# Kernel optimization log

Hardware: AMD Instinct MI355X
Metric: run time of the kernel (lower is better)

The kernel has to match this reference:

```python
import jax, jax.numpy as jnp
import numpy as np

# Layer sizes for each 3-layer LSTM tower (input_dim, hidden_dim), as in the torch module.
SIZES = [(50, 25), (25, 10), (10, 4)]
B = 32768


def _lstm(x, Wih, Whh, b):
    """Single-layer batch-first LSTM (torch gate order i,f,g,o). x: [B,T,Din].
    Returns (ys [B,T,H], h_last [B,H]). b = b_ih + b_hh combined."""
    Bn = x.shape[0]
    H = Whh.shape[1]

    def step(carry, xt):
        h, c = carry
        gates = xt @ Wih.T + h @ Whh.T + b  # [B, 4H]
        i, f, g, o = jnp.split(gates, 4, axis=-1)
        c = jax.nn.sigmoid(f) * c + jax.nn.sigmoid(i) * jnp.tanh(g)
        h = jax.nn.sigmoid(o) * jnp.tanh(c)
        return (h, c), h

    z = jnp.zeros((Bn, H), x.dtype)
    (h_last, _), ys = jax.lax.scan(step, (z, z), jnp.swapaxes(x, 0, 1))
    return jnp.swapaxes(ys, 0, 1), h_last


def _tower(x, params):
    h = None
    for (Wih, Whh, b) in params:
        x, h = _lstm(x, Wih, Whh, b)
    return h  # last layer's final hidden state [B, 4]


def setup_inputs() -> dict:
    key = jax.random.key(0)
    inp = {}
    k_q, k_p, key = jax.random.split(key, 3)
    inp["q"] = jax.random.normal(k_q, (B, 12, 50), jnp.float32)
    inp["p"] = jax.random.normal(k_p, (B, 50, 50), jnp.float32)
    for prefix in ("q", "p"):
        for i, (din, dh) in enumerate(SIZES):
            k1, k2, key = jax.random.split(key, 3)
            inp[f"{prefix}Wih{i}"] = jax.random.normal(k1, (4 * dh, din), jnp.float32) * (1.0 / np.sqrt(din))
            inp[f"{prefix}Whh{i}"] = jax.random.normal(k2, (4 * dh, dh), jnp.float32) * (1.0 / np.sqrt(dh))
            inp[f"{prefix}b{i}"] = jnp.zeros((4 * dh,), jnp.float32)
    k1, key = jax.random.split(key)
    inp["fW"] = jax.random.normal(k1, (2, 4), jnp.float32) * 0.5
    inp["fb"] = jnp.zeros((2,), jnp.float32)
    return inp


def reference(q, p,
              qWih0, qWhh0, qb0, qWih1, qWhh1, qb1, qWih2, qWhh2, qb2,
              pWih0, pWhh0, pb0, pWih1, pWhh1, pb1, pWih2, pWhh2, pb2,
              fW, fb):
    q_params = [(qWih0, qWhh0, qb0), (qWih1, qWhh1, qb1), (qWih2, qWhh2, qb2)]
    p_params = [(pWih0, pWhh0, pb0), (pWih1, pWhh1, pb1), (pWih2, pWhh2, pb2)]
    h_q = _tower(q, q_params)  # [B, 4]
    h_p = _tower(p, p_params)  # [B, 4]
    scores = h_q * h_p
    return jax.nn.softmax(scores @ fW.T + fb, axis=1)  # [B, 2]
```

## Files before the change

kernel.cpp:

```cpp
#include <hip/hip_runtime.h>
#include <cstddef>

#define DEV static __device__ __forceinline__

constexpr int B_TOTAL = 32768;
constexpr int ROWS = 128;
constexpr int NBLK = B_TOTAL / ROWS;

constexpr int WL1_OFF = 7800, WL2_OFF = 9400, W_TOTAL = 9656;
constexpr int H0_STR = 28;
constexpr int H1_STR = 12;
constexpr int HQ_OFF = 0;
constexpr int HP_OFF = B_TOTAL * 4;

DEV float fexp2(float x) { return __builtin_amdgcn_exp2f(x); }
DEV float frcp(float x) { return __builtin_amdgcn_rcpf(x); }
DEV float fsig(float x) { return frcp(1.0f + fexp2(-1.4426950408889634f * x)); }
DEV float ftanh_(float x) { return 2.0f * frcp(1.0f + fexp2(-2.8853900817779268f * x)) - 1.0f; }

DEV float elem4(const float4 v, const int jj) {
  return jj == 0 ? v.x : jj == 1 ? v.y : jj == 2 ? v.z : v.w;
}

template <int NU>
DEV void gfma(float* __restrict__ g0, float* __restrict__ g1,
              const float4* __restrict__ w, const float va, const float vb) {
#pragma unroll
  for (int u = 0; u < NU; ++u) {
    const float4 wv = w[u];
    g0[4 * u + 0] = fmaf(wv.x, va, g0[4 * u + 0]);
    g0[4 * u + 1] = fmaf(wv.y, va, g0[4 * u + 1]);
    g0[4 * u + 2] = fmaf(wv.z, va, g0[4 * u + 2]);
    g0[4 * u + 3] = fmaf(wv.w, va, g0[4 * u + 3]);
    g1[4 * u + 0] = fmaf(wv.x, vb, g1[4 * u + 0]);
    g1[4 * u + 1] = fmaf(wv.y, vb, g1[4 * u + 1]);
    g1[4 * u + 2] = fmaf(wv.z, vb, g1[4 * u + 2]);
    g1[4 * u + 3] = fmaf(wv.w, vb, g1[4 * u + 3]);
  }
}

template <int NU>
DEV void activ(const float* __restrict__ g, float* __restrict__ c,
               float* __restrict__ hn) {
#pragma unroll
  for (int u = 0; u < NU; ++u) {
    const float gi_ = fsig(g[4 * u + 0]);
    const float gf  = fsig(g[4 * u + 1]);
    const float gg  = ftanh_(g[4 * u + 2]);
    const float go  = fsig(g[4 * u + 3]);
    const float cn  = fmaf(gf, c[u], gi_ * gg);
    c[u] = cn;
    hn[u] = go * ftanh_(cn);
  }
}

template <int NU>
DEV void l0_fw(const float* __restrict__ wl, const float* __restrict__ bia,
               const float* __restrict__ xa, const float* __restrict__ xb,
               const float* h0, const int ra, const int rb, const int u0,
               float* __restrict__ c, float* __restrict__ hn) {
  float g0[4 * NU], g1[4 * NU];
#pragma unroll
  for (int k = 0; k < 4 * NU; ++k) { g0[k] = bia[k]; g1[k] = bia[k]; }

#pragma unroll 5
  for (int m = 0; m < 25; ++m) {
    const float2 a2 = *reinterpret_cast<const float2*>(xa + 2 * m);
    const float2 b2 = *reinterpret_cast<const float2*>(xb + 2 * m);
    const float4* w0 = reinterpret_cast<const float4*>(wl + (2 * m) * 100) + u0;
    const float4* w1 = reinterpret_cast<const float4*>(wl + (2 * m + 1) * 100) + u0;
    gfma<NU>(g0, g1, w0, a2.x, b2.x);
    gfma<NU>(g0, g1, w1, a2.y, b2.y);
  }
#pragma unroll
  for (int gi = 0; gi < 7; ++gi) {
    const float4 ha = *reinterpret_cast<const float4*>(h0 + ra * H0_STR + 4 * gi);
    const float4 hb = *reinterpret_cast<const float4*>(h0 + rb * H0_STR + 4 * gi);
#pragma unroll
    for (int jj = 0; jj < 4; ++jj) {
      const float4* w = reinterpret_cast<const float4*>(wl + (50 + 4 * gi + jj) * 100) + u0;
      gfma<NU>(g0, g1, w, elem4(ha, jj), elem4(hb, jj));
    }
  }
  activ<NU>(g0, c, hn);
  activ<NU>(g1, c + 4, hn + 4);
}

template <int NU>
DEV void l1_fw(const float* __restrict__ wl, const float* __restrict__ bia,
               const float* h0, const float* h1, const int ra, const int rb,
               const int u0, float* __restrict__ c, float* __restrict__ hn) {
  float g0[4 * NU], g1[4 * NU];
#pragma unroll
  for (int k = 0; k < 4 * NU; ++k) { g0[k] = bia[k]; g1[k] = bia[k]; }
#pragma unroll
  for (int gi = 0; gi < 7; ++gi) {
    const float4 ha = *reinterpret_cast<const float4*>(h0 + ra * H0_STR + 4 * gi);
    const float4 hb = *reinterpret_cast<const float4*>(h0 + rb * H0_STR + 4 * gi);
#pragma unroll
    for (int jj = 0; jj < 4; ++jj) {
      const float4* w = reinterpret_cast<const float4*>(wl + (4 * gi + jj) * 40) + u0;
      gfma<NU>(g0, g1, w, elem4(ha, jj), elem4(hb, jj));
    }
  }
#pragma unroll
  for (int gi = 0; gi < 3; ++gi) {
    const float4 ha = *reinterpret_cast<const float4*>(h1 + ra * H1_STR + 4 * gi);
    const float4 hb = *reinterpret_cast<const float4*>(h1 + rb * H1_STR + 4 * gi);
#pragma unroll
    for (int jj = 0; jj < 4; ++jj) {
      const float4* w = reinterpret_cast<const float4*>(wl + (28 + 4 * gi + jj) * 40) + u0;
      gfma<NU>(g0, g1, w, elem4(ha, jj), elem4(hb, jj));
    }
  }
  activ<NU>(g0, c, hn);
  activ<NU>(g1, c + 2, hn + 2);
}

DEV void l2_fw(const float* __restrict__ wl, const float* __restrict__ bi2,
               const float* h1, const int ra, const int rb,
               float* __restrict__ c, float* __restrict__ h2) {
  float g0[16], g1[16];
#pragma unroll
  for (int k = 0; k < 16; ++k) { g0[k] = bi2[k]; g1[k] = bi2[k]; }
#pragma unroll
  for (int gi = 0; gi < 3; ++gi) {
    const float4 ha = *reinterpret_cast<const float4*>(h1 + ra * H1_STR + 4 * gi);
    const float4 hb = *reinterpret_cast<const float4*>(h1 + rb * H1_STR + 4 * gi);
#pragma unroll
    for (int jj = 0; jj < 4; ++jj) {
      const float4* w = reinterpret_cast<const float4*>(wl + (4 * gi + jj) * 16);
      gfma<4>(g0, g1, w, elem4(ha, jj), elem4(hb, jj));
    }
  }
#pragma unroll
  for (int jj = 0; jj < 4; ++jj) {
    const float4* w = reinterpret_cast<const float4*>(wl + (12 + jj) * 16);
    gfma<4>(g0, g1, w, h2[jj], h2[4 + jj]);
  }
  activ<4>(g0, c, h2);
  activ<4>(g1, c + 4, h2 + 4);
}

__global__ __launch_bounds__(512, 2) void lstm_towers(
    const float* __restrict__ q, const float* __restrict__ p,
    const float* __restrict__ qWih0, const float* __restrict__ qWhh0, const float* __restrict__ qb0,
    const float* __restrict__ qWih1, const float* __restrict__ qWhh1, const float* __restrict__ qb1,
    const float* __restrict__ qWih2, const float* __restrict__ qWhh2, const float* __restrict__ qb2,
    const float* __restrict__ pWih0, const float* __restrict__ pWhh0, const float* __restrict__ pb0,
    const float* __restrict__ pWih1, const float* __restrict__ pWhh1, const float* __restrict__ pb1,
    const float* __restrict__ pWih2, const float* __restrict__ pWhh2, const float* __restrict__ pb2,
    float* __restrict__ hq_out, float* __restrict__ hp_out) {
  __shared__ float wlds[W_TOTAL];
  __shared__ float h0s[ROWS * H0_STR];
  __shared__ float h1s[2 * ROWS * H1_STR];

  const int tid = threadIdx.x;
  const int r = tid & 63;
  const int wid = tid >> 6;
  const int row0 = blockIdx.x * ROWS;
  const int ra = r, rb = r + 64;

  const int u00 = __builtin_amdgcn_readfirstlane(
      wid < 2 ? 4 * wid : (wid < 7 ? 8 + 3 * (wid - 2) : 23));
  const int u01 = __builtin_amdgcn_readfirstlane(wid < 2 ? 2 * wid : wid + 2);

  const float* wl0 = wlds;
  const float* wl1 = wlds + WL1_OFF;
  const float* wl2 = wlds + WL2_OFF;

#pragma unroll 1
  for (int phase = 0; phase < 2; ++phase) {
    const bool isp = (phase == 1);
    const float* __restrict__ x = isp ? p : q;
    const int T = isp ? 50 : 12;
    const float* Wih0 = isp ? pWih0 : qWih0; const float* Whh0 = isp ? pWhh0 : qWhh0;
    const float* b0g  = isp ? pb0   : qb0;
    const float* Wih1 = isp ? pWih1 : qWih1; const float* Whh1 = isp ? pWhh1 : qWhh1;
    const float* b1g  = isp ? pb1   : qb1;
    const float* Wih2 = isp ? pWih2 : qWih2; const float* Whh2 = isp ? pWhh2 : qWhh2;
    const float* b2g  = isp ? pb2   : qb2;
    float* __restrict__ hout_g = isp ? hp_out : hq_out;

    __syncthreads();

    for (int e = tid; e < W_TOTAL; e += 512) {
      float v = 0.0f;
      if (e < WL1_OFF) {
        const int j = e / 100, k = e % 100, u = k >> 2, gt = k & 3, rr = gt * 25 + u;
        if (j < 50) v = Wih0[rr * 50 + j];
        else { const int jh = j - 50; if (jh < 25) v = Whh0[rr * 25 + jh]; }
      } else if (e < WL2_OFF) {
        const int i = e - WL1_OFF, j = i / 40, k = i % 40, u = k >> 2, gt = k & 3;
        const int rr = gt * 10 + u;
        if (j < 25) v = Wih1[rr * 25 + j];
        else if (j >= 28) { const int jh = j - 28; if (jh < 10) v = Whh1[rr * 10 + jh]; }
      } else {
        const int i = e - WL2_OFF, j = i / 16, k = i % 16, u = k >> 2, gt = k & 3;
        const int rr = gt * 4 + u;
        if (j < 10) v = Wih2[rr * 10 + j];
        else if (j >= 12) v = Whh2[rr * 4 + (j - 12)];
      }
      wlds[e] = v;
    }
    for (int i = tid; i < ROWS * H0_STR; i += 512) h0s[i] = 0.0f;
    for (int i = tid; i < 2 * ROWS * H1_STR; i += 512) h1s[i] = 0.0f;

    float bia0[16], bia1[8], bi2[16];
#pragma unroll
    for (int u = 0; u < 4; ++u) {
      const int ui = (u00 + u < 25) ? u00 + u : 24;
#pragma unroll
      for (int gt = 0; gt < 4; ++gt) bia0[4 * u + gt] = b0g[gt * 25 + ui];
    }
#pragma unroll
    for (int u = 0; u < 2; ++u) {
      const int ui = (u01 + u < 10) ? u01 + u : 9;
#pragma unroll
      for (int gt = 0; gt < 4; ++gt) bia1[4 * u + gt] = b1g[gt * 10 + ui];
    }
    if (wid == 7) {
#pragma unroll
      for (int u = 0; u < 4; ++u)
#pragma unroll
        for (int gt = 0; gt < 4; ++gt) bi2[4 * u + gt] = b2g[gt * 4 + u];
    }

    float c0[8] = {}, hn0[8];
    float c1[4] = {}, hn1[4];
    float c2[8] = {}, h2r[8] = {};

    const float* xa = x + (size_t)(row0 + ra) * T * 50;
    const float* xb = x + (size_t)(row0 + rb) * T * 50;

    __syncthreads();

    int s = 0;
#pragma unroll 1
    for (int t = 0; t < T; ++t) {
      if (wid < 2)      l0_fw<4>(wl0, bia0, xa, xb, h0s, ra, rb, u00, c0, hn0);
      else if (wid < 7) l0_fw<3>(wl0, bia0, xa, xb, h0s, ra, rb, u00, c0, hn0);
      else              l0_fw<2>(wl0, bia0, xa, xb, h0s, ra, rb, u00, c0, hn0);
      __syncthreads();
      {
        float* da = &h0s[ra * H0_STR + u00];
        float* db = &h0s[rb * H0_STR + u00];
        if (wid < 2) {
          da[0] = hn0[0]; da[1] = hn0[1]; da[2] = hn0[2]; da[3] = hn0[3];
          db[0] = hn0[4]; db[1] = hn0[5]; db[2] = hn0[6]; db[3] = hn0[7];
        } else if (wid < 7) {
          da[0] = hn0[0]; da[1] = hn0[1]; da[2] = hn0[2];
          db[0] = hn0[4]; db[1] = hn0[5]; db[2] = hn0[6];
        } else {
          da[0] = hn0[0]; da[1] = hn0[1];
          db[0] = hn0[4]; db[1] = hn0[5];
        }
      }
      __syncthreads();
      const float* h1rd = h1s + s * (ROWS * H1_STR);
      float* h1wr = h1s + (s ^ 1) * (ROWS * H1_STR);
      if (wid < 2) l1_fw<2>(wl1, bia1, h0s, h1rd, ra, rb, u01, c1, hn1);
      else         l1_fw<1>(wl1, bia1, h0s, h1rd, ra, rb, u01, c1, hn1);
      {
        float* ea = &h1wr[ra * H1_STR + u01];
        float* eb = &h1wr[rb * H1_STR + u01];
        if (wid < 2) { ea[0] = hn1[0]; ea[1] = hn1[1]; eb[0] = hn1[2]; eb[1] = hn1[3]; }
        else         { ea[0] = hn1[0]; eb[0] = hn1[2]; }
      }
      __syncthreads();
      if (wid == 7) l2_fw(wl2, bi2, h1wr, ra, rb, c2, h2r);
      s ^= 1;
      xa += 50; xb += 50;
    }
    if (wid == 7) {
      reinterpret_cast<float4*>(hout_g)[row0 + ra] =
          make_float4(h2r[0], h2r[1], h2r[2], h2r[3]);
      reinterpret_cast<float4*>(hout_g)[row0 + rb] =
          make_float4(h2r[4], h2r[5], h2r[6], h2r[7]);
    }
  }
}

__global__ __launch_bounds__(256) void combine_head(
    const float* __restrict__ hq, const float* __restrict__ hp,
    const float* __restrict__ fW, const float* __restrict__ fb,
    float* __restrict__ out) {
  const int b = blockIdx.x * blockDim.x + (int)threadIdx.x;
  if (b >= B_TOTAL) return;
  const float4 vq = reinterpret_cast<const float4*>(hq)[b];
  const float4 vp = reinterpret_cast<const float4*>(hp)[b];
  const float s0 = vq.x * vp.x, s1 = vq.y * vp.y, s2 = vq.z * vp.z, s3 = vq.w * vp.w;
  float l0 = fb[0], l1 = fb[1];
  l0 = fmaf(s0, fW[0], l0); l0 = fmaf(s1, fW[1], l0); l0 = fmaf(s2, fW[2], l0); l0 = fmaf(s3, fW[3], l0);
  l1 = fmaf(s0, fW[4], l1); l1 = fmaf(s1, fW[5], l1); l1 = fmaf(s2, fW[6], l1); l1 = fmaf(s3, fW[7], l1);
  const float m = fmaxf(l0, l1);
  const float e0 = fexp2(1.4426950408889634f * (l0 - m));
  const float e1 = fexp2(1.4426950408889634f * (l1 - m));
  const float inv = frcp(e0 + e1);
  reinterpret_cast<float2*>(out)[b] = make_float2(e0 * inv, e1 * inv);
}

extern "C" void kernel_launch(void* const* d_in, const int* in_sizes, int n_in,
                              void* d_out, int out_size, void* d_ws, size_t ws_size,
                              hipStream_t stream) {
  (void)in_sizes; (void)n_in; (void)out_size; (void)ws_size;
  const float* q = (const float*)d_in[0];
  const float* p = (const float*)d_in[1];
  float* ws = (float*)d_ws;

  lstm_towers<<<NBLK, 512, 0, stream>>>(
      q, p,
      (const float*)d_in[2], (const float*)d_in[3], (const float*)d_in[4],
      (const float*)d_in[5], (const float*)d_in[6], (const float*)d_in[7],
      (const float*)d_in[8], (const float*)d_in[9], (const float*)d_in[10],
      (const float*)d_in[11], (const float*)d_in[12], (const float*)d_in[13],
      (const float*)d_in[14], (const float*)d_in[15], (const float*)d_in[16],
      (const float*)d_in[17], (const float*)d_in[18], (const float*)d_in[19],
      ws + HQ_OFF, ws + HP_OFF);

  combine_head<<<B_TOTAL / 256, 256, 0, stream>>>(
      ws + HQ_OFF, ws + HP_OFF,
      (const float*)d_in[20], (const float*)d_in[21], (float*)d_out);
}
```

Baseline: 1.360 ms.

## Process two timesteps of layer-0 input projection per weight load

Unrolls the time loop by two so the layer-0 input projection for steps t and t+1 is computed together. Each weight float4 loaded from LDS is then reused across four row/time accumulators, which halves LDS weight traffic for the input part. Biases are moved into LDS padding slots instead of per-thread registers. Layer-1 work is remapped onto warps 2-7 so warps 0-1 are freed. The cost is higher register pressure from the extra accumulators, and T must be even.

```diff
diff --git a/kernel.cpp b/kernel.cpp
--- a/kernel.cpp
+++ b/kernel.cpp
@@ -23,8 +23,8 @@
 }
 
 template <int NU>
-DEV void gfma(float* __restrict__ g0, float* __restrict__ g1,
-              const float4* __restrict__ w, const float va, const float vb) {
+DEV void gfma1(float* __restrict__ g0, float* __restrict__ g1,
+               const float4* __restrict__ w, const float va, const float vb) {
 #pragma unroll
   for (int u = 0; u < NU; ++u) {
     const float4 wv = w[u];
@@ -40,6 +40,33 @@
 }
 
 template <int NU>
+DEV void gfma2(float* __restrict__ a0, float* __restrict__ a1,
+               float* __restrict__ b0, float* __restrict__ b1,
+               const float4* __restrict__ w,
+               const float xat, const float xbt, const float xan, const float xbn) {
+#pragma unroll
+  for (int u = 0; u < NU; ++u) {
+    const float4 wv = w[u];
+    a0[4 * u + 0] = fmaf(wv.x, xat, a0[4 * u + 0]);
+    a0[4 * u + 1] = fmaf(wv.y, xat, a0[4 * u + 1]);
+    a0[4 * u + 2] = fmaf(wv.z, xat, a0[4 * u + 2]);
+    a0[4 * u + 3] = fmaf(wv.w, xat, a0[4 * u + 3]);
+    a1[4 * u + 0] = fmaf(wv.x, xbt, a1[4 * u + 0]);
+    a1[4 * u + 1] = fmaf(wv.y, xbt, a1[4 * u + 1]);
+    a1[4 * u + 2] = fmaf(wv.z, xbt, a1[4 * u + 2]);
+    a1[4 * u + 3] = fmaf(wv.w, xbt, a1[4 * u + 3]);
+    b0[4 * u + 0] = fmaf(wv.x, xan, b0[4 * u + 0]);
+    b0[4 * u + 1] = fmaf(wv.y, xan, b0[4 * u + 1]);
+    b0[4 * u + 2] = fmaf(wv.z, xan, b0[4 * u + 2]);
+    b0[4 * u + 3] = fmaf(wv.w, xan, b0[4 * u + 3]);
+    b1[4 * u + 0] = fmaf(wv.x, xbn, b1[4 * u + 0]);
+    b1[4 * u + 1] = fmaf(wv.y, xbn, b1[4 * u + 1]);
+    b1[4 * u + 2] = fmaf(wv.z, xbn, b1[4 * u + 2]);
+    b1[4 * u + 3] = fmaf(wv.w, xbn, b1[4 * u + 3]);
+  }
+}
+
+template <int NU>
 DEV void activ(const float* __restrict__ g, float* __restrict__ c,
                float* __restrict__ hn) {
 #pragma unroll
@@ -55,88 +82,132 @@
 }
 
 template <int NU>
-DEV void l0_fw(const float* __restrict__ wl, const float* __restrict__ bia,
-               const float* __restrict__ xa, const float* __restrict__ xb,
-               const float* h0, const int ra, const int rb, const int u0,
-               float* __restrict__ c, float* __restrict__ hn) {
-  float g0[4 * NU], g1[4 * NU];
-#pragma unroll
-  for (int k = 0; k < 4 * NU; ++k) { g0[k] = bia[k]; g1[k] = bia[k]; }
-
-#pragma unroll 5
+DEV void l0_even(const float* __restrict__ wl,
+                 const float* __restrict__ x2a, const float* __restrict__ x2b,
+                 const float* h0, const int ra, const int rb, const int u0,
+                 float* __restrict__ c, float* __restrict__ hn,
+                 float* __restrict__ gb0, float* __restrict__ gb1) {
+  float ga0[4 * NU], ga1[4 * NU];
+  {
+    const float4* bq = reinterpret_cast<const float4*>(wl + 7700) + u0;
+#pragma unroll
+    for (int u = 0; u < NU; ++u) {
+      const float4 b = bq[u];
+      ga0[4 * u + 0] = b.x; ga0[4 * u + 1] = b.y; ga0[4 * u + 2] = b.z; ga0[4 * u + 3] = b.w;
+      ga1[4 * u + 0] = b.x; ga1[4 * u + 1] = b.y; ga1[4 * u + 2] = b.z; ga1[4 * u + 3] = b.w;
+      gb0[4 * u + 0] = b.x; gb0[4 * u + 1] = b.y; gb0[4 * u + 2] = b.z; gb0[4 * u + 3] = b.w;
+      gb1[4 * u + 0] = b.x; gb1[4 * u + 1] = b.y; gb1[4 * u + 2] = b.z; gb1[4 * u + 3] = b.w;
+    }
+  }
+#pragma unroll 2
   for (int m = 0; m < 25; ++m) {
-    const float2 a2 = *reinterpret_cast<const float2*>(xa + 2 * m);
-    const float2 b2 = *reinterpret_cast<const float2*>(xb + 2 * m);
+    const float2 at = *reinterpret_cast<const float2*>(x2a + 2 * m);
+    const float2 an = *reinterpret_cast<const float2*>(x2a + 50 + 2 * m);
+    const float2 bt = *reinterpret_cast<const float2*>(x2b + 2 * m);
+    const float2 bn = *reinterpret_cast<const float2*>(x2b + 50 + 2 * m);
     const float4* w0 = reinterpret_cast<const float4*>(wl + (2 * m) * 100) + u0;
     const float4* w1 = reinterpret_cast<const float4*>(wl + (2 * m + 1) * 100) + u0;
-    gfma<NU>(g0, g1, w0, a2.x, b2.x);
-    gfma<NU>(g0, g1, w1, a2.y, b2.y);
-  }
-#pragma unroll
+    gfma2<NU>(ga0, ga1, gb0, gb1, w0, at.x, bt.x, an.x, bn.x);
+    gfma2<NU>(ga0, ga1, gb0, gb1, w1, at.y, bt.y, an.y, bn.y);
+  }
+#pragma unroll 1
   for (int gi = 0; gi < 7; ++gi) {
     const float4 ha = *reinterpret_cast<const float4*>(h0 + ra * H0_STR + 4 * gi);
     const float4 hb = *reinterpret_cast<const float4*>(h0 + rb * H0_STR + 4 * gi);
 #pragma unroll
     for (int jj = 0; jj < 4; ++jj) {
       const float4* w = reinterpret_cast<const float4*>(wl + (50 + 4 * gi + jj) * 100) + u0;
-      gfma<NU>(g0, g1, w, elem4(ha, jj), elem4(hb, jj));
-    }
-  }
-  activ<NU>(g0, c, hn);
-  activ<NU>(g1, c + 4, hn + 4);
-}
-
-template <int NU>
-DEV void l1_fw(const float* __restrict__ wl, const float* __restrict__ bia,
-               const float* h0, const float* h1, const int ra, const int rb,
-               const int u0, float* __restrict__ c, float* __restrict__ hn) {
-  float g0[4 * NU], g1[4 * NU];
-#pragma unroll
-  for (int k = 0; k < 4 * NU; ++k) { g0[k] = bia[k]; g1[k] = bia[k]; }
-#pragma unroll
+      gfma1<NU>(ga0, ga1, w, elem4(ha, jj), elem4(hb, jj));
+    }
+  }
+  activ<NU>(ga0, c, hn);
+  activ<NU>(ga1, c + 4, hn + 4);
+}
+
+template <int NU>
+DEV void l0_odd(const float* __restrict__ wl, const float* h0,
+                const int ra, const int rb, const int u0,
+                float* __restrict__ c, float* __restrict__ hn,
+                float* __restrict__ g0, float* __restrict__ g1) {
+#pragma unroll 1
   for (int gi = 0; gi < 7; ++gi) {
     const float4 ha = *reinterpret_cast<const float4*>(h0 + ra * H0_STR + 4 * gi);
     const float4 hb = *reinterpret_cast<const float4*>(h0 + rb * H0_STR + 4 * gi);
 #pragma unroll
     for (int jj = 0; jj < 4; ++jj) {
+      const float4* w = reinterpret_cast<const float4*>(wl + (50 + 4 * gi + jj) * 100) + u0;
+      gfma1<NU>(g0, g1, w, elem4(ha, jj), elem4(hb, jj));
+    }
+  }
+  activ<NU>(g0, c, hn);
+  activ<NU>(g1, c + 4, hn + 4);
+}
+
+template <int NU>
+DEV void l1_fw(const float* __restrict__ wl, const float* h0, const float* h1,
+               const int ra, const int rb, const int u0,
+               float* __restrict__ c, float* __restrict__ hn) {
+  float g0[4 * NU], g1[4 * NU];
+  {
+    const float4* bq = reinterpret_cast<const float4*>(wl + 1560) + u0;
+#pragma unroll
+    for (int u = 0; u < NU; ++u) {
+      const float4 b = bq[u];
+      g0[4 * u + 0] = b.x; g0[4 * u + 1] = b.y; g0[4 * u + 2] = b.z; g0[4 * u + 3] = b.w;
+      g1[4 * u + 0] = b.x; g1[4 * u + 1] = b.y; g1[4 * u + 2] = b.z; g1[4 * u + 3] = b.w;
+    }
+  }
+#pragma unroll 1
+  for (int gi = 0; gi < 7; ++gi) {
+    const float4 ha = *reinterpret_cast<const float4*>(h0 + ra * H0_STR + 4 * gi);
+    const float4 hb = *reinterpret_cast<const float4*>(h0 + rb * H0_STR + 4 * gi);
+#pragma unroll
+    for (int jj = 0; jj < 4; ++jj) {
       const float4* w = reinterpret_cast<const float4*>(wl + (4 * gi + jj) * 40) + u0;
-      gfma<NU>(g0, g1, w, elem4(ha, jj), elem4(hb, jj));
-    }
-  }
-#pragma unroll
+      gfma1<NU>(g0, g1, w, elem4(ha, jj), elem4(hb, jj));
+    }
+  }
+#pragma unroll 1
   for (int gi = 0; gi < 3; ++gi) {
     const float4 ha = *reinterpret_cast<const float4*>(h1 + ra * H1_STR + 4 * gi);
     const float4 hb = *reinterpret_cast<const float4*>(h1 + rb * H1_STR + 4 * gi);
 #pragma unroll
     for (int jj = 0; jj < 4; ++jj) {
       const float4* w = reinterpret_cast<const float4*>(wl + (28 + 4 * gi + jj) * 40) + u0;
-      gfma<NU>(g0, g1, w, elem4(ha, jj), elem4(hb, jj));
+      gfma1<NU>(g0, g1, w, elem4(ha, jj), elem4(hb, jj));
     }
   }
   activ<NU>(g0, c, hn);
   activ<NU>(g1, c + 2, hn + 2);
 }
 
-DEV void l2_fw(const float* __restrict__ wl, const float* __restrict__ bi2,
-               const float* h1, const int ra, const int rb,
-               float* __restrict__ c, float* __restrict__ h2) {
+DEV void l2_fw(const float* __restrict__ wl, const float* h1,
+               const int ra, const int rb, float* __restrict__ c,
+               float* __restrict__ h2) {
   float g0[16], g1[16];
-#pragma unroll
-  for (int k = 0; k < 16; ++k) { g0[k] = bi2[k]; g1[k] = bi2[k]; }
-#pragma unroll
+  {
+    const float4* bq = reinterpret_cast<const float4*>(wl + 176);
+#pragma unroll
+    for (int u = 0; u < 4; ++u) {
+      const float4 b = bq[u];
+      g0[4 * u + 0] = b.x; g0[4 * u + 1] = b.y; g0[4 * u + 2] = b.z; g0[4 * u + 3] = b.w;
+      g1[4 * u + 0] = b.x; g1[4 * u + 1] = b.y; g1[4 * u + 2] = b.z; g1[4 * u + 3] = b.w;
+    }
+  }
+#pragma unroll 1
   for (int gi = 0; gi < 3; ++gi) {
     const float4 ha = *reinterpret_cast<const float4*>(h1 + ra * H1_STR + 4 * gi);
     const float4 hb = *reinterpret_cast<const float4*>(h1 + rb * H1_STR + 4 * gi);
 #pragma unroll
     for (int jj = 0; jj < 4; ++jj) {
       const float4* w = reinterpret_cast<const float4*>(wl + (4 * gi + jj) * 16);
-      gfma<4>(g0, g1, w, elem4(ha, jj), elem4(hb, jj));
+      gfma1<4>(g0, g1, w, elem4(ha, jj), elem4(hb, jj));
     }
   }
 #pragma unroll
   for (int jj = 0; jj < 4; ++jj) {
     const float4* w = reinterpret_cast<const float4*>(wl + (12 + jj) * 16);
-    gfma<4>(g0, g1, w, h2[jj], h2[4 + jj]);
+    gfma1<4>(g0, g1, w, h2[jj], h2[4 + jj]);
   }
   activ<4>(g0, c, h2);
   activ<4>(g1, c + 4, h2 + 4);
@@ -163,7 +234,8 @@
 
   const int u00 = __builtin_amdgcn_readfirstlane(
       wid < 2 ? 4 * wid : (wid < 7 ? 8 + 3 * (wid - 2) : 23));
-  const int u01 = __builtin_amdgcn_readfirstlane(wid < 2 ? 2 * wid : wid + 2);
+  const int u01 = __builtin_amdgcn_readfirstlane(
+      wid < 6 ? 2 * (wid - 2) : 8 + (wid - 6));
 
   const float* wl0 = wlds;
   const float* wl1 = wlds + WL1_OFF;
@@ -189,16 +261,19 @@
       if (e < WL1_OFF) {
         const int j = e / 100, k = e % 100, u = k >> 2, gt = k & 3, rr = gt * 25 + u;
         if (j < 50) v = Wih0[rr * 50 + j];
-        else { const int jh = j - 50; if (jh < 25) v = Whh0[rr * 25 + jh]; }
+        else if (j < 75) v = Whh0[rr * 25 + (j - 50)];
+        else if (j == 77) v = b0g[gt * 25 + u];
       } else if (e < WL2_OFF) {
         const int i = e - WL1_OFF, j = i / 40, k = i % 40, u = k >> 2, gt = k & 3;
         const int rr = gt * 10 + u;
         if (j < 25) v = Wih1[rr * 25 + j];
-        else if (j >= 28) { const int jh = j - 28; if (jh < 10) v = Whh1[rr * 10 + jh]; }
+        else if (j >= 28 && j < 38) v = Whh1[rr * 10 + (j - 28)];
+        else if (j == 39) v = b1g[gt * 10 + u];
       } else {
         const int i = e - WL2_OFF, j = i / 16, k = i % 16, u = k >> 2, gt = k & 3;
         const int rr = gt * 4 + u;
         if (j < 10) v = Wih2[rr * 10 + j];
+        else if (j == 11) v = b2g[gt * 4 + u];
         else if (j >= 12) v = Whh2[rr * 4 + (j - 12)];
       }
       wlds[e] = v;
@@ -206,41 +281,22 @@
     for (int i = tid; i < ROWS * H0_STR; i += 512) h0s[i] = 0.0f;
     for (int i = tid; i < 2 * ROWS * H1_STR; i += 512) h1s[i] = 0.0f;
 
-    float bia0[16], bia1[8], bi2[16];
-#pragma unroll
-    for (int u = 0; u < 4; ++u) {
-      const int ui = (u00 + u < 25) ? u00 + u : 24;
-#pragma unroll
-      for (int gt = 0; gt < 4; ++gt) bia0[4 * u + gt] = b0g[gt * 25 + ui];
-    }
-#pragma unroll
-    for (int u = 0; u < 2; ++u) {
-      const int ui = (u01 + u < 10) ? u01 + u : 9;
-#pragma unroll
-      for (int gt = 0; gt < 4; ++gt) bia1[4 * u + gt] = b1g[gt * 10 + ui];
-    }
-    if (wid == 7) {
-#pragma unroll
-      for (int u = 0; u < 4; ++u)
-#pragma unroll
-        for (int gt = 0; gt < 4; ++gt) bi2[4 * u + gt] = b2g[gt * 4 + u];
-    }
-
     float c0[8] = {}, hn0[8];
     float c1[4] = {}, hn1[4];
     float c2[8] = {}, h2r[8] = {};
-
-    const float* xa = x + (size_t)(row0 + ra) * T * 50;
-    const float* xb = x + (size_t)(row0 + rb) * T * 50;
+    float gb0[16], gb1[16];
+
+    const float* x2a = x + (size_t)(row0 + ra) * T * 50;
+    const float* x2b = x + (size_t)(row0 + rb) * T * 50;
 
     __syncthreads();
 
     int s = 0;
 #pragma unroll 1
-    for (int t = 0; t < T; ++t) {
-      if (wid < 2)      l0_fw<4>(wl0, bia0, xa, xb, h0s, ra, rb, u00, c0, hn0);
-      else if (wid < 7) l0_fw<3>(wl0, bia0, xa, xb, h0s, ra, rb, u00, c0, hn0);
-      else              l0_fw<2>(wl0, bia0, xa, xb, h0s, ra, rb, u00, c0, hn0);
+    for (int tp = 0; tp < T; tp += 2) {
+      if (wid < 2)      l0_even<4>(wl0, x2a, x2b, h0s, ra, rb, u00, c0, hn0, gb0, gb1);
+      else if (wid < 7) l0_even<3>(wl0, x2a, x2b, h0s, ra, rb, u00, c0, hn0, gb0, gb1);
+      else              l0_even<2>(wl0, x2a, x2b, h0s, ra, rb, u00, c0, hn0, gb0, gb1);
       __syncthreads();
       {
         float* da = &h0s[ra * H0_STR + u00];
@@ -257,20 +313,56 @@
         }
       }
       __syncthreads();
-      const float* h1rd = h1s + s * (ROWS * H1_STR);
-      float* h1wr = h1s + (s ^ 1) * (ROWS * H1_STR);
-      if (wid < 2) l1_fw<2>(wl1, bia1, h0s, h1rd, ra, rb, u01, c1, hn1);
-      else         l1_fw<1>(wl1, bia1, h0s, h1rd, ra, rb, u01, c1, hn1);
       {
-        float* ea = &h1wr[ra * H1_STR + u01];
-        float* eb = &h1wr[rb * H1_STR + u01];
-        if (wid < 2) { ea[0] = hn1[0]; ea[1] = hn1[1]; eb[0] = hn1[2]; eb[1] = hn1[3]; }
-        else         { ea[0] = hn1[0]; eb[0] = hn1[2]; }
+        const float* h1rd = h1s + s * (ROWS * H1_STR);
+        float* h1wr = h1s + (s ^ 1) * (ROWS * H1_STR);
+        if (wid >= 2 && wid < 6) l1_fw<2>(wl1, h0s, h1rd, ra, rb, u01, c1, hn1);
+        else if (wid >= 6)       l1_fw<1>(wl1, h0s, h1rd, ra, rb, u01, c1, hn1);
+        if (wid >= 2) {
+          float* ea = &h1wr[ra * H1_STR + u01];
+          float* eb = &h1wr[rb * H1_STR + u01];
+          if (wid < 6) { ea[0] = hn1[0]; ea[1] = hn1[1]; eb[0] = hn1[2]; eb[1] = hn1[3]; }
+          else         { ea[0] = hn1[0]; eb[0] = hn1[2]; }
+        }
+        __syncthreads();
+        if (wid == 7) l2_fw(wl2, h1wr, ra, rb, c2, h2r);
+      }
+      s ^= 1;
+      if (wid < 2)      l0_odd<4>(wl0, h0s, ra, rb, u00, c0, hn0, gb0, gb1);
+      else if (wid < 7) l0_odd<3>(wl0, h0s, ra, rb, u00, c0, hn0, gb0, gb1);
+      else              l0_odd<2>(wl0, h0s, ra, rb, u00, c0, hn0, gb0, gb1);
+      __syncthreads();
+      {
+        float* da = &h0s[ra * H0_STR + u00];
+        float* db = &h0s[rb * H0_STR + u00];
+        if (wid < 2) {
+          da[0] = hn0[0]; da[1] = hn0[1]; da[2] = hn0[2]; da[3] = hn0[3];
+          db[0] = hn0[4]; db[1] = hn0[5]; db[2] = hn0[6]; db[3] = hn0[7];
+        } else if (wid < 7) {
+          da[0] = hn0[0]; da[1] = hn0[1]; da[2] = hn0[2];
+          db[0] = hn0[4]; db[1] = hn0[5]; db[2] = hn0[6];
+        } else {
+          da[0] = hn0[0]; da[1] = hn0[1];
+          db[0] = hn0[4]; db[1] = hn0[5];
+        }
       }
       __syncthreads();
-      if (wid == 7) l2_fw(wl2, bi2, h1wr, ra, rb, c2, h2r);
+      {
+        const float* h1rd = h1s + s * (ROWS * H1_STR);
+        float* h1wr = h1s + (s ^ 1) * (ROWS * H1_STR);
+        if (wid >= 2 && wid < 6) l1_fw<2>(wl1, h0s, h1rd, ra, rb, u01, c1, hn1);
+        else if (wid >= 6)       l1_fw<1>(wl1, h0s, h1rd, ra, rb, u01, c1, hn1);
+        if (wid >= 2) {
+          float* ea = &h1wr[ra * H1_STR + u01];
+          float* eb = &h1wr[rb * H1_STR + u01];
+          if (wid < 6) { ea[0] = hn1[0]; ea[1] = hn1[1]; eb[0] = hn1[2]; eb[1] = hn1[3]; }
+          else         { ea[0] = hn1[0]; eb[0] = hn1[2]; }
+        }
+        __syncthreads();
+        if (wid == 7) l2_fw(wl2, h1wr, ra, rb, c2, h2r);
+      }
       s ^= 1;
-      xa += 50; xb += 50;
+      x2a += 100; x2b += 100;
     }
     if (wid == 7) {
       reinterpret_cast<float4*>(hout_g)[row0 + ra] =
```

After: 1.589 ms. 16.9% more time.
